# Performance work log

Measured on AMD Instinct MI355X. Metric: run time of the kernel, lower is better.

## Reference

```python
import jax, jax.numpy as jnp
import numpy as np

GAMMA = 0.5
NUM_NODES = 100000  # upper bound on node ids in edge_index


def setup_inputs() -> dict:
    key = jax.random.key(0)
    k1, k2 = jax.random.split(key)
    E = 6400000
    mask = jax.random.uniform(k1, (E, 1), dtype=jnp.float32)
    edge_index = jax.random.randint(k2, (2, E), 0, NUM_NODES, dtype=jnp.int64)
    return {"mask": mask, "edge_index": edge_index, "assign_edge": 1}


def _scatter_mean(vals, idx, num_segments):
    # torch_scatter mean: sum / clamp(count, min=1)
    sums = jax.ops.segment_sum(vals, idx, num_segments=num_segments)
    cnt = jax.ops.segment_sum(jnp.ones_like(vals), idx, num_segments=num_segments)
    return sums / jnp.maximum(cnt, 1.0)


def reference(mask, edge_index, assign_edge):
    src, dst = edge_index[0], edge_index[1]
    if assign_edge:
        # per-node mean of incident edge masks, then average endpoints per edge
        avg_node_mask = _scatter_mean(mask.reshape(-1), src, NUM_NODES)  # [N]
        smoothed = (avg_node_mask[src] + avg_node_mask[dst]) / 2  # [E]
    else:
        avg_edge_mask = (mask[src] + mask[dst]) / 2  # mask is per-node here
        smoothed = _scatter_mean(avg_edge_mask.reshape(-1), src, NUM_NODES)
    smoothed = smoothed.reshape((-1, 1))
    return (1.0 - GAMMA) * mask + GAMMA * smoothed
```

## Files before the change

kernel.cpp:

```cpp
#include <hip/hip_runtime.h>

#define NUM_NODES 100000
#define GAMMA 0.5f

typedef int   nint4   __attribute__((ext_vector_type(4)));
typedef float nfloat4 __attribute__((ext_vector_type(4)));
typedef unsigned short nushort8 __attribute__((ext_vector_type(8)));

#define SCALE 16384.0f
#define INV_SCALE (1.0f / 16384.0f)
#define CNT_ONE (1u << 22)
#define SUM_MASK ((1u << 22) - 1)

#define SCALE16 32768.0f
#define INV_SCALE16 (1.0f / 32768.0f)

#define NPART3 33334
#define NPART4 25000
#define NPART8 12500
#define NPARTH 25000


__global__ void __launch_bounds__(1024)
part_scatter3_kernel(const float* __restrict__ mask,
                     const int* __restrict__ src,
                     unsigned* __restrict__ partials,
                     int E, int CS, int C) {
    extern __shared__ unsigned tab[];
    const int g = blockIdx.x;
    const int cpx = C >> 3;
    const int xcd = g & 7;
    const int j = g >> 3;
    const int c = xcd * cpx + (j % cpx);
    const int p = j / cpx;
    const int pbase = p * NPART3;
    const int plen = min(NPART3, NUM_NODES - pbase);

    for (int t = threadIdx.x; t < plen; t += blockDim.x) tab[t] = 0u;
    __syncthreads();

    const int start = c * CS;
    const int end = min(E, start + CS);
    const int nquads = (end - start) >> 2;

    for (int q = threadIdx.x; q < nquads; q += blockDim.x) {
        const int i = start + q * 4;
        nint4 s = *(const nint4*)(src + i);
        nfloat4 m = *(const nfloat4*)(mask + i);
        int sx = s.x - pbase;
        if ((unsigned)sx < (unsigned)plen) atomicAdd(&tab[sx], CNT_ONE | (unsigned)(m.x * SCALE + 0.5f));
        int sy = s.y - pbase;
        if ((unsigned)sy < (unsigned)plen) atomicAdd(&tab[sy], CNT_ONE | (unsigned)(m.y * SCALE + 0.5f));
        int sz = s.z - pbase;
        if ((unsigned)sz < (unsigned)plen) atomicAdd(&tab[sz], CNT_ONE | (unsigned)(m.z * SCALE + 0.5f));
        int sw = s.w - pbase;
        if ((unsigned)sw < (unsigned)plen) atomicAdd(&tab[sw], CNT_ONE | (unsigned)(m.w * SCALE + 0.5f));
    }
    for (int i = start + nquads * 4 + threadIdx.x; i < end; i += blockDim.x) {
        int sx = src[i] - pbase;
        if ((unsigned)sx < (unsigned)plen)
            atomicAdd(&tab[sx], CNT_ONE | (unsigned)(mask[i] * SCALE + 0.5f));
    }

    __syncthreads();
    unsigned* dstp = partials + (size_t)c * NUM_NODES + pbase;
    for (int t = threadIdx.x; t < plen; t += blockDim.x)
        dstp[t] = tab[t];
}

__global__ void __launch_bounds__(1024)
part_scatter4_kernel(const float* __restrict__ mask,
                     const int* __restrict__ src,
                     unsigned* __restrict__ partials,
                     int E, int CS, int C) {
    extern __shared__ unsigned tab[];
    const int g = blockIdx.x;
    const int cpx = C >> 3;
    const int xcd = g & 7;
    const int j = g >> 3;
    const int c = xcd * cpx + (j % cpx);
    const int p = j / cpx;
    const int pbase = p * NPART4;

    for (int t = threadIdx.x; t < NPART4; t += blockDim.x) tab[t] = 0u;
    __syncthreads();

    const int start = c * CS;
    const int end = min(E, start + CS);
    const int nquads = (end - start) >> 2;

    for (int q = threadIdx.x; q < nquads; q += blockDim.x) {
        const int i = start + q * 4;
        nint4 s = *(const nint4*)(src + i);
        nfloat4 m = *(const nfloat4*)(mask + i);
        int sx = s.x - pbase;
        if ((unsigned)sx < NPART4) atomicAdd(&tab[sx], CNT_ONE | (unsigned)(m.x * SCALE + 0.5f));
        int sy = s.y - pbase;
        if ((unsigned)sy < NPART4) atomicAdd(&tab[sy], CNT_ONE | (unsigned)(m.y * SCALE + 0.5f));
        int sz = s.z - pbase;
        if ((unsigned)sz < NPART4) atomicAdd(&tab[sz], CNT_ONE | (unsigned)(m.z * SCALE + 0.5f));
        int sw = s.w - pbase;
        if ((unsigned)sw < NPART4) atomicAdd(&tab[sw], CNT_ONE | (unsigned)(m.w * SCALE + 0.5f));
    }
    for (int i = start + nquads * 4 + threadIdx.x; i < end; i += blockDim.x) {
        int sx = src[i] - pbase;
        if ((unsigned)sx < NPART4)
            atomicAdd(&tab[sx], CNT_ONE | (unsigned)(mask[i] * SCALE + 0.5f));
    }

    __syncthreads();
    unsigned* dstp = partials + (size_t)c * NUM_NODES + pbase;
    for (int t = threadIdx.x; t < NPART4; t += blockDim.x)
        dstp[t] = tab[t];
}

__global__ void __launch_bounds__(1024)
part_scatter8_kernel(const float* __restrict__ mask,
                     const int* __restrict__ src,
                     unsigned* __restrict__ partials,
                     int E, int CS, int C) {
    __shared__ unsigned tab[NPART8];
    const int g = blockIdx.x;
    const int cpx = C >> 3;
    const int xcd = g & 7;
    const int j = g >> 3;
    const int c = xcd * cpx + (j % cpx);
    const int p = j / cpx;
    const int pbase = p * NPART8;

    for (int t = threadIdx.x; t < NPART8; t += blockDim.x) tab[t] = 0u;
    __syncthreads();

    const int start = c * CS;
    const int end = min(E, start + CS);
    const int nquads = (end - start) >> 2;

    for (int q = threadIdx.x; q < nquads; q += blockDim.x) {
        const int i = start + q * 4;
        nint4 s = *(const nint4*)(src + i);
        nfloat4 m = *(const nfloat4*)(mask + i);
        int sx = s.x - pbase;
        if ((unsigned)sx < NPART8) atomicAdd(&tab[sx], CNT_ONE | (unsigned)(m.x * SCALE + 0.5f));
        int sy = s.y - pbase;
        if ((unsigned)sy < NPART8) atomicAdd(&tab[sy], CNT_ONE | (unsigned)(m.y * SCALE + 0.5f));
        int sz = s.z - pbase;
        if ((unsigned)sz < NPART8) atomicAdd(&tab[sz], CNT_ONE | (unsigned)(m.z * SCALE + 0.5f));
        int sw = s.w - pbase;
        if ((unsigned)sw < NPART8) atomicAdd(&tab[sw], CNT_ONE | (unsigned)(m.w * SCALE + 0.5f));
    }
    for (int i = start + nquads * 4 + threadIdx.x; i < end; i += blockDim.x) {
        int sx = src[i] - pbase;
        if ((unsigned)sx < NPART8)
            atomicAdd(&tab[sx], CNT_ONE | (unsigned)(mask[i] * SCALE + 0.5f));
    }

    __syncthreads();
    unsigned* dstp = partials + (size_t)c * NUM_NODES + pbase;
    for (int t = threadIdx.x; t < NPART8; t += blockDim.x)
        dstp[t] = tab[t];
}

__global__ void reduce_avg_kernel(const unsigned* __restrict__ partials,
                                  unsigned short* __restrict__ avgh,
                                  unsigned char* __restrict__ avgb,
                                  int C) {
    int n = blockIdx.x * blockDim.x + threadIdx.x;
    if (n < NUM_NODES) {
        unsigned cnt = 0, sum = 0;
#pragma unroll 8
        for (int c = 0; c < C; ++c) {
            unsigned v = __builtin_nontemporal_load(partials + (size_t)c * NUM_NODES + n);
            cnt += v >> 22;
            sum += v & SUM_MASK;
        }
        float a = ((float)sum * INV_SCALE) / fmaxf((float)cnt, 1.0f);
        avgh[n] = (unsigned short)(a * SCALE16 + 0.5f);
        avgb[n] = (unsigned char)(a * 255.0f + 0.5f);
    }
}

__global__ void __launch_bounds__(1024)
smooth_u8_kernel(const float* __restrict__ mask,
                 const int* __restrict__ src,
                 const int* __restrict__ dst,
                 const unsigned char* __restrict__ avgb,
                 float* __restrict__ out,
                 int E) {
    extern __shared__ unsigned char tabb[];
    const int t = (int)threadIdx.x;
    const int q0 = (int)blockIdx.x * 4096 + t;
    const int b0 = q0 * 4;
    const int b1 = b0 + 4096;
    const int b2 = b0 + 8192;
    const int b3 = b0 + 12288;
    const bool a0 = (b0 + 3 < E);
    const bool a1 = (b1 + 3 < E);
    const bool a2 = (b2 + 3 < E);
    const bool a3 = (b3 + 3 < E);

    nint4 s0, d0, s1, d1, s2, d2, s3, d3;
    if (a0) { s0 = __builtin_nontemporal_load((const nint4*)(src + b0));
              d0 = __builtin_nontemporal_load((const nint4*)(dst + b0)); }
    if (a1) { s1 = __builtin_nontemporal_load((const nint4*)(src + b1));
              d1 = __builtin_nontemporal_load((const nint4*)(dst + b1)); }
    if (a2) { s2 = __builtin_nontemporal_load((const nint4*)(src + b2));
              d2 = __builtin_nontemporal_load((const nint4*)(dst + b2)); }
    if (a3) { s3 = __builtin_nontemporal_load((const nint4*)(src + b3));
              d3 = __builtin_nontemporal_load((const nint4*)(dst + b3)); }

    const nint4* avg16 = (const nint4*)avgb;
    nint4* tab16 = (nint4*)tabb;
    for (int j = t; j < 6250; j += 1024)
        tab16[j] = avg16[j];
    __syncthreads();

    const float k = GAMMA * 0.5f * (1.0f / 255.0f);
#define SMOOTH_QUAD(an, sn, dn, bn)                                          \
    if (an) {                                                                \
        nfloat4 m = __builtin_nontemporal_load((const nfloat4*)(mask + bn)); \
        int ax = (int)tabb[sn.x] + (int)tabb[dn.x];                          \
        int ay = (int)tabb[sn.y] + (int)tabb[dn.y];                          \
        int az = (int)tabb[sn.z] + (int)tabb[dn.z];                          \
        int aw = (int)tabb[sn.w] + (int)tabb[dn.w];                          \
        nfloat4 o;                                                           \
        o.x = (1.0f - GAMMA) * m.x + k * (float)ax;                          \
        o.y = (1.0f - GAMMA) * m.y + k * (float)ay;                          \
        o.z = (1.0f - GAMMA) * m.z + k * (float)az;                          \
        o.w = (1.0f - GAMMA) * m.w + k * (float)aw;                          \
        __builtin_nontemporal_store(o, (nfloat4*)(out + bn));                \
    } else if (bn < E) {                                                     \
        for (int i = bn; i < E; ++i)                                         \
            out[i] = (1.0f - GAMMA) * mask[i] +                              \
                     GAMMA * 0.5f * ((float)avgb[src[i]] + (float)avgb[dst[i]]) * (1.0f / 255.0f); \
    }
    SMOOTH_QUAD(a0, s0, d0, b0)
    SMOOTH_QUAD(a1, s1, d1, b1)
    SMOOTH_QUAD(a2, s2, d2, b2)
    SMOOTH_QUAD(a3, s3, d3, b3)
#undef SMOOTH_QUAD
}

__global__ void __launch_bounds__(1024)
smooth_lds16x2_kernel(const float* __restrict__ mask,
                      const int* __restrict__ src,
                      const int* __restrict__ dst,
                      const unsigned short* __restrict__ avgh,
                      float* __restrict__ out,
                      int E) {
    __shared__ unsigned short tabh[NPARTH];
    const int t = (int)threadIdx.x;
    const int q0 = (int)blockIdx.x * 2048 + t;
    const int q1 = q0 + 1024;
    const int b0 = q0 * 4;
    const int b1 = q1 * 4;
    const bool a0 = (b0 + 3 < E);
    const bool a1 = (b1 + 3 < E);

    nint4 s0, d0, s1, d1;
    nfloat4 acc0, acc1;
    acc0.x = 0.0f; acc0.y = 0.0f; acc0.z = 0.0f; acc0.w = 0.0f;
    acc1.x = 0.0f; acc1.y = 0.0f; acc1.z = 0.0f; acc1.w = 0.0f;
    if (a0) { s0 = *(const nint4*)(src + b0); d0 = *(const nint4*)(dst + b0); }
    if (a1) { s1 = *(const nint4*)(src + b1); d1 = *(const nint4*)(dst + b1); }

    const nushort8* avg8 = (const nushort8*)avgh;
    nushort8* tab8 = (nushort8*)tabh;
    for (int p = 0; p < 4; ++p) {
        const int pbase = p * NPARTH;
        for (int j = t; j < NPARTH / 8; j += 1024)
            tab8[j] = avg8[(NPARTH / 8) * p + j];
        __syncthreads();
        int a;
        if (a0) {
            a = s0.x - pbase; if ((unsigned)a < NPARTH) acc0.x += (float)tabh[a];
            a = d0.x - pbase; if ((unsigned)a < NPARTH) acc0.x += (float)tabh[a];
            a = s0.y - pbase; if ((unsigned)a < NPARTH) acc0.y += (float)tabh[a];
            a = d0.y - pbase; if ((unsigned)a < NPARTH) acc0.y += (float)tabh[a];
            a = s0.z - pbase; if ((unsigned)a < NPARTH) acc0.z += (float)tabh[a];
            a = d0.z - pbase; if ((unsigned)a < NPARTH) acc0.z += (float)tabh[a];
            a = s0.w - pbase; if ((unsigned)a < NPARTH) acc0.w += (float)tabh[a];
            a = d0.w - pbase; if ((unsigned)a < NPARTH) acc0.w += (float)tabh[a];
        }
        if (a1) {
            a = s1.x - pbase; if ((unsigned)a < NPARTH) acc1.x += (float)tabh[a];
            a = d1.x - pbase; if ((unsigned)a < NPARTH) acc1.x += (float)tabh[a];
            a = s1.y - pbase; if ((unsigned)a < NPARTH) acc1.y += (float)tabh[a];
            a = d1.y - pbase; if ((unsigned)a < NPARTH) acc1.y += (float)tabh[a];
            a = s1.z - pbase; if ((unsigned)a < NPARTH) acc1.z += (float)tabh[a];
            a = d1.z - pbase; if ((unsigned)a < NPARTH) acc1.z += (float)tabh[a];
            a = s1.w - pbase; if ((unsigned)a < NPARTH) acc1.w += (float)tabh[a];
            a = d1.w - pbase; if ((unsigned)a < NPARTH) acc1.w += (float)tabh[a];
        }
        __syncthreads();
    }

    const float k = GAMMA * 0.5f * INV_SCALE16;
    if (a0) {
        nfloat4 m = *(const nfloat4*)(mask + b0);
        nfloat4 o;
        o.x = (1.0f - GAMMA) * m.x + k * acc0.x;
        o.y = (1.0f - GAMMA) * m.y + k * acc0.y;
        o.z = (1.0f - GAMMA) * m.z + k * acc0.z;
        o.w = (1.0f - GAMMA) * m.w + k * acc0.w;
        __builtin_nontemporal_store(o, (nfloat4*)(out + b0));
    } else if (b0 < E) {
        for (int i = b0; i < E; ++i)
            out[i] = (1.0f - GAMMA) * mask[i] +
                     GAMMA * 0.5f * ((float)avgh[src[i]] + (float)avgh[dst[i]]) * INV_SCALE16;
    }
    if (a1) {
        nfloat4 m = *(const nfloat4*)(mask + b1);
        nfloat4 o;
        o.x = (1.0f - GAMMA) * m.x + k * acc1.x;
        o.y = (1.0f - GAMMA) * m.y + k * acc1.y;
        o.z = (1.0f - GAMMA) * m.z + k * acc1.z;
        o.w = (1.0f - GAMMA) * m.w + k * acc1.w;
        __builtin_nontemporal_store(o, (nfloat4*)(out + b1));
    } else if (b1 < E) {
        for (int i = b1; i < E; ++i)
            out[i] = (1.0f - GAMMA) * mask[i] +
                     GAMMA * 0.5f * ((float)avgh[src[i]] + (float)avgh[dst[i]]) * INV_SCALE16;
    }
}


#define FIX_SCALE64 16777216.0f
#define SUM_MASK64 0xFFFFFFFFFFULL
#define CNT_ONE64 (1ULL << 40)

__global__ void scatter_sum_kernel(const float* __restrict__ mask,
                                   const int* __restrict__ src,
                                   unsigned long long* __restrict__ acc,
                                   int E) {
    int i4 = blockIdx.x * blockDim.x + threadIdx.x;
    int base = i4 * 4;
    if (base + 3 < E) {
        nint4 s = *(const nint4*)(src + base);
        nfloat4 m = *(const nfloat4*)(mask + base);
        atomicAdd(&acc[s.x], CNT_ONE64 | (unsigned long long)(unsigned)(m.x * FIX_SCALE64 + 0.5f));
        atomicAdd(&acc[s.y], CNT_ONE64 | (unsigned long long)(unsigned)(m.y * FIX_SCALE64 + 0.5f));
        atomicAdd(&acc[s.z], CNT_ONE64 | (unsigned long long)(unsigned)(m.z * FIX_SCALE64 + 0.5f));
        atomicAdd(&acc[s.w], CNT_ONE64 | (unsigned long long)(unsigned)(m.w * FIX_SCALE64 + 0.5f));
    } else {
        for (int i = base; i < E; ++i) {
            atomicAdd(&acc[src[i]],
                      CNT_ONE64 | (unsigned long long)(unsigned)(mask[i] * FIX_SCALE64 + 0.5f));
        }
    }
}

__global__ void avg_kernel(const unsigned long long* __restrict__ acc,
                           unsigned short* __restrict__ avgh,
                           unsigned char* __restrict__ avgb,
                           int N) {
    int i = blockIdx.x * blockDim.x + threadIdx.x;
    if (i < N) {
        unsigned long long pk = acc[i];
        float cnt = (float)(unsigned)(pk >> 40);
        float sum = (float)(pk & SUM_MASK64) * (1.0f / FIX_SCALE64);
        float a = sum / fmaxf(cnt, 1.0f);
        avgh[i] = (unsigned short)(a * SCALE16 + 0.5f);
        avgb[i] = (unsigned char)(a * 255.0f + 0.5f);
    }
}


static bool optin_lds(const void* fn, int bytes) {
    if (hipFuncSetAttribute(fn, hipFuncAttributeMaxDynamicSharedMemorySize,
                            bytes) != hipSuccess) return false;
    hipFuncAttributes fa;
    return hipFuncGetAttributes(&fa, fn) == hipSuccess &&
           fa.maxDynamicSharedSizeBytes >= bytes;
}

extern "C" void kernel_launch(void* const* d_in, const int* in_sizes, int n_in,
                              void* d_out, int out_size, void* d_ws, size_t ws_size,
                              hipStream_t stream) {
    const float* mask = (const float*)d_in[0];
    const int* edge_index = (const int*)d_in[1];
    const int E = in_sizes[0];
    const int* src = edge_index;
    const int* dstp = edge_index + E;
    float* out = (float*)d_out;

    const int B = 256;
    const int QTOT = (E + 3) / 4;
    const int GB3 = (QTOT + 4095) / 4096;
    const int GB2 = (QTOT + 2047) / 2048;

    const int lds3 = NPART3 * (int)sizeof(unsigned);
    const int lds4 = NPART4 * (int)sizeof(unsigned);
    const int ldsB = NUM_NODES;
    const bool use3 = optin_lds((const void*)part_scatter3_kernel, lds3);
    const bool use4 = use3 ? false
                           : optin_lds((const void*)part_scatter4_kernel, lds4);
    const bool useB = optin_lds((const void*)smooth_u8_kernel, ldsB);

    const size_t avg_bytes = (size_t)NUM_NODES * (sizeof(unsigned short) + 1);
    const size_t chunk_bytes = (size_t)NUM_NODES * sizeof(unsigned);
    const int CMAX = use3 ? 80 : 64;
    int C = 0;
    if (ws_size > avg_bytes + chunk_bytes) {
        C = (int)((ws_size - avg_bytes) / chunk_bytes);
        if (C > CMAX) C = CMAX;
        C &= ~7;
    }

    if (C >= 16) {
        unsigned* partials = (unsigned*)d_ws;
        unsigned short* avgh = (unsigned short*)((char*)d_ws + (size_t)C * chunk_bytes);
        unsigned char* avgb = (unsigned char*)(avgh + NUM_NODES);
        int CS = (((E + C - 1) / C) + 3) & ~3;

        if (use3 && C == 80) {
            part_scatter3_kernel<<<C * 3, 1024, lds3, stream>>>(mask, src, partials, E, CS, C);
        } else if (use3 || use4) {
            if (!use4) (void)optin_lds((const void*)part_scatter4_kernel, lds4);
            part_scatter4_kernel<<<C * 4, 1024, lds4, stream>>>(mask, src, partials, E, CS, C);
        } else {
            part_scatter8_kernel<<<C * 8, 1024, 0, stream>>>(mask, src, partials, E, CS, C);
        }
        reduce_avg_kernel<<<(NUM_NODES + B - 1) / B, B, 0, stream>>>(partials, avgh, avgb, C);
        if (useB) {
            smooth_u8_kernel<<<GB3, 1024, ldsB, stream>>>(mask, src, dstp, avgb, out, E);
        } else {
            smooth_lds16x2_kernel<<<GB2, 1024, 0, stream>>>(mask, src, dstp, avgh, out, E);
        }
    } else {
        unsigned long long* acc = (unsigned long long*)d_ws;
        unsigned short* avgh = (unsigned short*)(acc + NUM_NODES);
        unsigned char* avgb = (unsigned char*)(avgh + NUM_NODES);
        (void)hipMemsetAsync(d_ws, 0, NUM_NODES * sizeof(unsigned long long), stream);
        scatter_sum_kernel<<<(QTOT + B - 1) / B, B, 0, stream>>>(mask, src, acc, E);
        avg_kernel<<<(NUM_NODES + B - 1) / B, B, 0, stream>>>(acc, avgh, avgb, NUM_NODES);
        if (useB) {
            smooth_u8_kernel<<<GB3, 1024, ldsB, stream>>>(mask, src, dstp, avgb, out, E);
        } else {
            smooth_lds16x2_kernel<<<GB2, 1024, 0, stream>>>(mask, src, dstp, avgh, out, E);
        }
    }
}
```

Baseline: 140.9 us.

## Pack per-node count and sum into 16-bit LDS slots to halve partition passes

Adds a scatter path that packs a 4-bit edge count and a 12-bit quantized mask sum into 16-bit slots, two per 32-bit LDS word. Half the nodes now fit per block, so each edge chunk is scanned twice instead of three times. It uses 128 chunks with 16-bit partials and a matching reduce kernel. The price is coarser mask quantization (1/256) and possible field overflow if a node receives many edges within one chunk.

```diff
diff --git a/kernel.cpp b/kernel.cpp
--- a/kernel.cpp
+++ b/kernel.cpp
@@ -12,14 +12,88 @@
 #define CNT_ONE (1u << 22)
 #define SUM_MASK ((1u << 22) - 1)
 
+#define CNT16 (1u << 12)
+#define SUM16_MASK 0xFFFu
+
 #define SCALE16 32768.0f
 #define INV_SCALE16 (1.0f / 32768.0f)
 
+#define NPART2 50000
 #define NPART3 33334
 #define NPART4 25000
 #define NPART8 12500
 #define NPARTH 25000
 
+
+__global__ void __launch_bounds__(1024)
+part_scatter2_kernel(const float* __restrict__ mask,
+                     const int* __restrict__ src,
+                     unsigned short* __restrict__ partials2,
+                     int E, int CS, int C) {
+    extern __shared__ unsigned tab32[];
+    const int g = blockIdx.x;
+    const int cpx = C >> 3;
+    const int xcd = g & 7;
+    const int j = g >> 3;
+    const int c = xcd * cpx + (j % cpx);
+    const int p = j / cpx;
+    const int pbase = p * NPART2;
+
+    for (int t = threadIdx.x; t < NPART2 / 2; t += blockDim.x) tab32[t] = 0u;
+    __syncthreads();
+
+    const int start = c * CS;
+    const int end = min(E, start + CS);
+    const int nquads = (end - start) >> 2;
+
+    for (int q = threadIdx.x; q < nquads; q += blockDim.x) {
+        const int i = start + q * 4;
+        nint4 s = *(const nint4*)(src + i);
+        nfloat4 m = *(const nfloat4*)(mask + i);
+        int l;
+        l = s.x - pbase;
+        if ((unsigned)l < NPART2)
+            atomicAdd(&tab32[l >> 1], (CNT16 | (unsigned)(m.x * 256.0f + 0.5f)) << ((l & 1) * 16));
+        l = s.y - pbase;
+        if ((unsigned)l < NPART2)
+            atomicAdd(&tab32[l >> 1], (CNT16 | (unsigned)(m.y * 256.0f + 0.5f)) << ((l & 1) * 16));
+        l = s.z - pbase;
+        if ((unsigned)l < NPART2)
+            atomicAdd(&tab32[l >> 1], (CNT16 | (unsigned)(m.z * 256.0f + 0.5f)) << ((l & 1) * 16));
+        l = s.w - pbase;
+        if ((unsigned)l < NPART2)
+            atomicAdd(&tab32[l >> 1], (CNT16 | (unsigned)(m.w * 256.0f + 0.5f)) << ((l & 1) * 16));
+    }
+    for (int i = start + nquads * 4 + threadIdx.x; i < end; i += blockDim.x) {
+        int l = src[i] - pbase;
+        if ((unsigned)l < NPART2)
+            atomicAdd(&tab32[l >> 1], (CNT16 | (unsigned)(mask[i] * 256.0f + 0.5f)) << ((l & 1) * 16));
+    }
+
+    __syncthreads();
+    unsigned* dstp = (unsigned*)(partials2 + (size_t)c * NUM_NODES + pbase);
+    for (int t = threadIdx.x; t < NPART2 / 2; t += blockDim.x)
+        dstp[t] = tab32[t];
+}
+
+__global__ void reduce_avg2_kernel(const unsigned short* __restrict__ partials2,
+                                   unsigned short* __restrict__ avgh,
+                                   unsigned char* __restrict__ avgb,
+                                   int C) {
+    int n = blockIdx.x * blockDim.x + threadIdx.x;
+    if (n < NUM_NODES) {
+        unsigned cnt = 0, sum = 0;
+#pragma unroll 8
+        for (int c = 0; c < C; ++c) {
+            unsigned v = __builtin_nontemporal_load(partials2 + (size_t)c * NUM_NODES + n);
+            cnt += v >> 12;
+            sum += v & SUM16_MASK;
+        }
+        float a = ((float)sum * (1.0f / 256.0f)) / fmaxf((float)cnt, 1.0f);
+        avgh[n] = (unsigned short)(a * SCALE16 + 0.5f);
+        avgb[n] = (unsigned char)(fminf(a, 1.0f) * 255.0f + 0.5f);
+    }
+}
 
 __global__ void __launch_bounds__(1024)
 part_scatter3_kernel(const float* __restrict__ mask,
@@ -388,15 +462,38 @@
     const int GB3 = (QTOT + 4095) / 4096;
     const int GB2 = (QTOT + 2047) / 2048;
 
+    const int lds2 = (NPART2 / 2) * (int)sizeof(unsigned);
     const int lds3 = NPART3 * (int)sizeof(unsigned);
     const int lds4 = NPART4 * (int)sizeof(unsigned);
     const int ldsB = NUM_NODES;
+    const bool useB = optin_lds((const void*)smooth_u8_kernel, ldsB);
+
+    const size_t avg_bytes = (size_t)NUM_NODES * (sizeof(unsigned short) + 1);
+
+    const int C2 = 128;
+    const size_t p2_bytes = (size_t)C2 * NUM_NODES * sizeof(unsigned short) + avg_bytes;
+    bool use2 = (E <= 16000000) && ws_size > p2_bytes &&
+                optin_lds((const void*)part_scatter2_kernel, lds2);
+
+    if (use2) {
+        unsigned short* partials2 = (unsigned short*)d_ws;
+        unsigned short* avgh = partials2 + (size_t)C2 * NUM_NODES;
+        unsigned char* avgb = (unsigned char*)(avgh + NUM_NODES);
+        int CS = (((E + C2 - 1) / C2) + 3) & ~3;
+
+        part_scatter2_kernel<<<C2 * 2, 1024, lds2, stream>>>(mask, src, partials2, E, CS, C2);
+        reduce_avg2_kernel<<<(NUM_NODES + B - 1) / B, B, 0, stream>>>(partials2, avgh, avgb, C2);
+        if (useB) {
+            smooth_u8_kernel<<<GB3, 1024, ldsB, stream>>>(mask, src, dstp, avgb, out, E);
+        } else {
+            smooth_lds16x2_kernel<<<GB2, 1024, 0, stream>>>(mask, src, dstp, avgh, out, E);
+        }
+        return;
+    }
+
     const bool use3 = optin_lds((const void*)part_scatter3_kernel, lds3);
     const bool use4 = use3 ? false
                            : optin_lds((const void*)part_scatter4_kernel, lds4);
-    const bool useB = optin_lds((const void*)smooth_u8_kernel, ldsB);
-
-    const size_t avg_bytes = (size_t)NUM_NODES * (sizeof(unsigned short) + 1);
     const size_t chunk_bytes = (size_t)NUM_NODES * sizeof(unsigned);
     const int CMAX = use3 ? 80 : 64;
     int C = 0;
```

Result: no change. 140.5 us (-0.3%).
